# Kernel optimization log

Measured on AMD Instinct MI355X. Metric: run time of the kernel, lower is better.

## Reference

```python
import jax, jax.numpy as jnp
import numpy as np

PI = float(np.pi)
C64 = jnp.complex64

# ---- gate matrices (PennyLane conventions) ----

def _rx(t):
    c = jnp.cos(t / 2); s = jnp.sin(t / 2)
    return jnp.array([[c, -1j * s], [-1j * s, c]]).astype(C64)

def _rz(t):
    return jnp.array([[jnp.exp(-0.5j * t), 0.0], [0.0, jnp.exp(0.5j * t)]]).astype(C64)

def _rot(phi, th, om):
    # Rot(phi, theta, omega) = RZ(omega) RY(theta) RZ(phi)
    c = jnp.cos(th / 2); s = jnp.sin(th / 2)
    return jnp.array([
        [jnp.exp(-0.5j * (phi + om)) * c, -jnp.exp(0.5j * (phi - om)) * s],
        [jnp.exp(-0.5j * (phi - om)) * s,  jnp.exp(0.5j * (phi + om)) * c],
    ]).astype(C64)

def _crx(t):
    c = jnp.cos(t / 2); s = jnp.sin(t / 2)
    return jnp.array([
        [1, 0, 0, 0],
        [0, 1, 0, 0],
        [0, 0, c, -1j * s],
        [0, 0, -1j * s, c],
    ]).astype(C64)

CNOT = jnp.array([[1, 0, 0, 0], [0, 1, 0, 0], [0, 0, 0, 1], [0, 0, 1, 0]], dtype=C64)

# ---- state-vector primitives (state shape (2,)*n) ----

def _ap1(psi, U, w):
    return jnp.moveaxis(jnp.tensordot(U, psi, axes=((1,), (w,))), 0, w)

def _ap2(psi, U, a, b):
    U = U.reshape(2, 2, 2, 2)
    return jnp.moveaxis(jnp.tensordot(U, psi, axes=((2, 3), (a, b))), (0, 1), (a, b))

def _expZ(psi, w):
    p = jnp.moveaxis(jnp.abs(psi) ** 2, w, 0)
    return (p[0] - p[1]).sum()

def _expX(psi, w):
    return jnp.real(jnp.sum(jnp.conj(psi) * jnp.flip(psi, axis=w)))

# wire pairs in initQKV_on_wires order
_PAIRS = [(0, 1), (1, 2), (2, 3), (3, 0), (0, 3), (1, 0), (2, 1), (3, 2)]

def _init_qkv(psi, rot_p, crx_p, off):
    for i, (a, b) in enumerate(_PAIRS):
        psi = _ap1(psi, _rot(rot_p[3 * i], rot_p[3 * i + 1], rot_p[3 * i + 2]), off + a)
        psi = _ap2(psi, _crx(crx_p[i]), off + a, off + b)
        psi = _ap2(psi, CNOT, off + a, off + b)
    return psi

def _sample(x, qr, qc, kr, kc, vr, vc):
    # qmha_score: 8-qubit circuit
    psi = jnp.zeros((2,) * 8, C64).at[(0,) * 8].set(1.0)
    for w in range(4):  # AngleEmbedding (RX) of xq
        psi = _ap1(psi, _rx(x[w]), w)
    psi = _init_qkv(psi, qr, qc, 0)
    for w in range(4):  # AngleEmbedding (RX) of xk (same x)
        psi = _ap1(psi, _rx(x[w]), w)
    psi = _init_qkv(psi, kr, kc, 4)
    for w in range(4):
        psi = _ap2(psi, CNOT, w, w + 4)
    z = jnp.stack([_expZ(psi, w) for w in range(4)])
    xm = jnp.stack([_expX(psi, w) for w in range(4)])
    score = jnp.sqrt(z * z + xm * xm)
    # qmha_value: 4-qubit circuit
    phi = jnp.zeros((2,) * 4, C64).at[(0,) * 4].set(1.0)
    for w in range(4):
        phi = _ap1(phi, _rx(x[w]), w)
    phi = _init_qkv(phi, vr, vc, 0)
    for w in range(4):
        phi = _ap1(phi, _rz(jnp.tanh(score[w]) * PI), w)
    for a, b in [(0, 1), (1, 2), (2, 3)]:
        phi = _ap2(phi, CNOT, a, b)
    zv = jnp.stack([_expZ(phi, w) for w in range(4)])
    xv = jnp.stack([_expX(phi, w) for w in range(4)])
    return jnp.concatenate([zv, xv])  # [8]


def setup_inputs() -> dict:
    key = jax.random.key(0)
    ks = jax.random.split(key, 12)
    B = 16384
    u = lambda k, n: jax.random.uniform(k, (n,), jnp.float32, -PI / 2, PI / 2)
    return {
        "x1": jax.random.normal(ks[0], (B, 96), jnp.float32),
        "pre_w": jax.random.normal(ks[1], (4, 96), jnp.float32) / np.sqrt(96.0),
        "pre_b": jnp.zeros((4,), jnp.float32),
        "q_rot": u(ks[2], 24),
        "k_rot": u(ks[3], 24),
        "v_rot": u(ks[4], 24),
        "q_crx": 0.1 * jax.random.normal(ks[5], (8,), jnp.float32),
        "k_crx": 0.1 * jax.random.normal(ks[6], (8,), jnp.float32),
        "v_crx": 0.1 * jax.random.normal(ks[7], (8,), jnp.float32),
        "ln_w": jnp.ones((8,), jnp.float32),
        "ln_b": jnp.zeros((8,), jnp.float32),
        "head_w": jax.random.normal(ks[8], (2, 8), jnp.float32) / np.sqrt(8.0),
        "head_b": jnp.zeros((2,), jnp.float32),
    }


def reference(x1, pre_w, pre_b, q_rot, k_rot, v_rot, q_crx, k_crx, v_crx,
              ln_w, ln_b, head_w, head_b):
    x = x1 @ pre_w.T + pre_b  # [B, 4] angles
    outs = jax.vmap(lambda xi: _sample(xi, q_rot, q_crx, k_rot, k_crx, v_rot, v_crx))(x)  # [B, 8]
    mu = outs.mean(-1, keepdims=True)
    var = outs.var(-1, keepdims=True)
    y = (outs - mu) / jnp.sqrt(var + 1e-5) * ln_w + ln_b  # LayerNorm(8)
    g = jax.nn.gelu(y, approximate=False)  # torch nn.GELU default = exact erf
    return g @ head_w.T + head_b  # [B, 2]
```

## Files before the change

kernel.cpp:

```cpp
#include <hip/hip_runtime.h>
#include <math.h>

#define PI_F 3.14159265358979323846f

struct c32 { float x, y; };

#define DPP_X1 0xB1
#define DPP_X2 0x4E
#define DPP_X3 0x1B

template<int CTRL>
__device__ __forceinline__ float dppf(float v){
  return __int_as_float(__builtin_amdgcn_update_dpp(
      0, __float_as_int(v), CTRL, 0xF, 0xF, true));
}

__device__ __forceinline__ float qred(float v){
  v += dppf<DPP_X1>(v);
  v += dppf<DPP_X2>(v);
  return v;
}

__device__ __forceinline__ float sel4(bool b0, bool b1,
                                      float v0, float v1, float v2, float v3){
  float lo = b0 ? v1 : v0;
  float hi = b0 ? v3 : v2;
  return b1 ? hi : lo;
}

__device__ __forceinline__ float fast_tanh(float x){
  float e = __expf(2.f * x);
  return 1.f - 2.f * __builtin_amdgcn_rcpf(e + 1.f);
}


template<int XM>
__device__ __forceinline__ void rot_lane(c32* a, float Ax, float Ay,
                                         float Cx, float Cy, float sgn){
  c32 r[4];
  #pragma unroll
  for (int k = 0; k < 4; k++){ r[k].x = dppf<XM>(a[k].x); r[k].y = dppf<XM>(a[k].y); }
  float Py = Ay * sgn, Qx = -Cx * sgn;
  #pragma unroll
  for (int k = 0; k < 4; k++){
    float nx = Ax*a[k].x - Py*a[k].y + Qx*r[k].x - Cy*r[k].y;
    float ny = Ax*a[k].y + Py*a[k].x + Qx*r[k].y + Cy*r[k].x;
    a[k].x = nx; a[k].y = ny;
  }
}

template<int MB>
__device__ __forceinline__ void rot_local(c32* a, float Ax, float Ay,
                                          float Cx, float Cy){
  #pragma unroll
  for (int k = 0; k < 4; k++){
    if (k & MB) continue;
    c32 u = a[k], v = a[k|MB];
    a[k].x    = Ax*u.x - Ay*u.y - Cx*v.x - Cy*v.y;
    a[k].y    = Ax*u.y + Ay*u.x - Cx*v.y + Cy*v.x;
    a[k|MB].x = Cx*u.x - Cy*u.y + Ax*v.x + Ay*v.y;
    a[k|MB].y = Cx*u.y + Cy*u.x + Ax*v.y - Ay*v.x;
  }
}

__device__ __forceinline__ void crx_pair(c32& u, c32& v, float c, float sn){
  c32 uo = u, vo = v;
  u.x = c*vo.x + sn*uo.y;  u.y = c*vo.y - sn*uo.x;
  v.x = c*uo.x + sn*vo.y;  v.y = c*uo.y - sn*vo.x;
}

template<int KM>
__device__ __forceinline__ void crx_lanectl_local(c32* a, float c, float sn, bool act){
  c32 n[4];
  #pragma unroll
  for (int k = 0; k < 4; k++){
    n[k].x = c*a[k^KM].x + sn*a[k].y;
    n[k].y = c*a[k^KM].y - sn*a[k].x;
  }
  #pragma unroll
  for (int k = 0; k < 4; k++){
    a[k].x = act ? n[k].x : a[k].x;
    a[k].y = act ? n[k].y : a[k].y;
  }
}

template<int XM, int K0, int K1>
__device__ __forceinline__ void crx_localctl_lane(c32* a, float c, float sn){
  float rx0 = dppf<XM>(a[K0].x), ry0 = dppf<XM>(a[K0].y);
  float rx1 = dppf<XM>(a[K1].x), ry1 = dppf<XM>(a[K1].y);
  float u0x = a[K0].x, u0y = a[K0].y, u1x = a[K1].x, u1y = a[K1].y;
  a[K0].x = c*rx0 + sn*u0y;  a[K0].y = c*ry0 - sn*u0x;
  a[K1].x = c*rx1 + sn*u1y;  a[K1].y = c*ry1 - sn*u1x;
}

template<int XM>
__device__ __forceinline__ void crx_lane_lane(c32* a, float c, float sn, bool act){
  #pragma unroll
  for (int k = 0; k < 4; k++){
    float rx = dppf<XM>(a[k].x), ry = dppf<XM>(a[k].y);
    float nx = c*rx + sn*a[k].y;
    float ny = c*ry - sn*a[k].x;
    a[k].x = act ? nx : a[k].x;
    a[k].y = act ? ny : a[k].y;
  }
}

__device__ __forceinline__ void sim4(c32* a, const float* __restrict__ gp,
                                     float sgnW0, float sgnW1, bool qb0, bool qb1){
  rot_lane<DPP_X2>(a, gp[0],  gp[1],  gp[2],  gp[3],  sgnW0);
  crx_lane_lane<DPP_X1>(a, gp[4], gp[5], qb1);
  rot_lane<DPP_X1>(a, gp[8],  gp[9],  gp[10], gp[11], sgnW1);
  crx_lanectl_local<2>(a, gp[12], gp[13], qb0);
  rot_local<2>(a, gp[16], gp[17], gp[18], gp[19]);
  crx_pair(a[2], a[3], gp[20], gp[21]);
  rot_local<1>(a, gp[24], gp[25], gp[26], gp[27]);
  crx_localctl_lane<DPP_X2,1,3>(a, gp[28], gp[29]);
  rot_lane<DPP_X2>(a, gp[32], gp[33], gp[34], gp[35], sgnW0);
  crx_lanectl_local<1>(a, gp[36], gp[37], qb1);
  rot_lane<DPP_X1>(a, gp[40], gp[41], gp[42], gp[43], sgnW1);
  crx_lane_lane<DPP_X2>(a, gp[44], gp[45], qb0);
  rot_local<2>(a, gp[48], gp[49], gp[50], gp[51]);
  crx_localctl_lane<DPP_X1,2,3>(a, gp[52], gp[53]);
  rot_local<1>(a, gp[56], gp[57], gp[58], gp[59]);
  crx_pair(a[1], a[3], gp[60], gp[61]);
}

__device__ __forceinline__ void build_rx4(c32* a, const float* cw, const float* sw,
                                          int q, bool qb0, bool qb1){
  float m01 = (qb1 ? sw[0] : cw[0]) * (qb0 ? sw[1] : cw[1]);
  float g0 = m01 * (cw[2]*cw[3]);
  float g1 = m01 * (cw[2]*sw[3]);
  float g2 = m01 * (sw[2]*cw[3]);
  float g3 = m01 * (sw[2]*sw[3]);
  float bx = (q == 0) ? 1.f : (q == 3) ? -1.f : 0.f;
  float by = (q == 1 || q == 2) ? -1.f : 0.f;
  a[0].x =  g0*bx;  a[0].y =  g0*by;
  a[1].x =  g1*by;  a[1].y = -g1*bx;
  a[2].x =  g2*by;  a[2].y = -g2*bx;
  a[3].x = -g3*bx;  a[3].y = -g3*by;
}

__device__ __forceinline__ void apply_rot_red16(c32* s, const int w,
                                                float Ax, float Ay, float Cx, float Cy){
  const int m = 8 >> w;
  #pragma unroll
  for (int i = 0; i < 16; i++){
    if (i & m) continue;
    c32 a = s[i], b = s[i | m];
    s[i].x     = Ax*a.x - Ay*a.y - Cx*b.x - Cy*b.y;
    s[i].y     = Ax*a.y + Ay*a.x - Cx*b.y + Cy*b.x;
    s[i | m].x = Cx*a.x - Cy*a.y + Ax*b.x + Ay*b.y;
    s[i | m].y = Cx*a.y + Cy*a.x + Ax*b.y - Ay*b.x;
  }
}

__device__ __forceinline__ void apply_crxnot16(c32* s, const int wa, const int wb,
                                               float c, float sn){
  const int ma = 8 >> wa, mb = 8 >> wb;
  #pragma unroll
  for (int i = 0; i < 16; i++){
    if (!(i & ma) || (i & mb)) continue;
    c32 u = s[i], v = s[i | mb];
    s[i]      = { c*v.x + sn*u.y, c*v.y - sn*u.x };
    s[i | mb] = { c*u.x + sn*v.y, c*u.y - sn*v.x };
  }
}

__global__ __launch_bounds__(64, 1) void qc_setup(
    const float* __restrict__ q_rot, const float* __restrict__ k_rot,
    const float* __restrict__ v_rot,
    const float* __restrict__ q_crx, const float* __restrict__ k_crx,
    const float* __restrict__ v_crx,
    float* __restrict__ ws){

  __shared__ float gates[3 * 64];
  const int t = threadIdx.x;

  if (t < 24){
    const int grp = t >> 3, g = t & 7;
    const float* rotp = grp == 0 ? q_rot : (grp == 1 ? k_rot : v_rot);
    const float* crxp = grp == 0 ? q_crx : (grp == 1 ? k_crx : v_crx);
    float phi = rotp[3*g], th = rotp[3*g+1], om = rotp[3*g+2];
    float c, s, ca, sa, cb, sb;
    __sincosf(0.5f*th,       &s,  &c);
    __sincosf(0.5f*(phi+om), &sa, &ca);
    __sincosf(0.5f*(phi-om), &sb, &cb);
    float cc, cs; __sincosf(0.5f*crxp[g], &cs, &cc);
    float* dst = &gates[64*grp + 8*g];
    dst[0] = c*ca; dst[1] = -c*sa; dst[2] = s*cb; dst[3] = -s*sb;
    dst[4] = cc;   dst[5] = cs;
    dst[6] = 0.f;  dst[7] = 0.f;
  }
  __syncthreads();

  c32 ks[16];
  #pragma unroll
  for (int i = 0; i < 16; i++) ks[i] = { 0.f, 0.f };
  ks[0] = { 1.f, 0.f };
  {
    constexpr int pa[8] = {0,1,2,3,0,1,2,3};
    constexpr int pb[8] = {1,2,3,0,3,0,1,2};
    #pragma unroll
    for (int g = 0; g < 8; g++){
      const float* qq = &gates[64 + 8*g];
      apply_rot_red16(ks, pa[g], qq[0], qq[1], qq[2], qq[3]);
      apply_crxnot16(ks, pa[g], pb[g], qq[4], qq[5]);
    }
  }
  float cxk[4];
  #pragma unroll
  for (int w = 0; w < 4; w++){
    const int m = 8 >> w;
    float r = 0.f;
    #pragma unroll
    for (int i = 0; i < 16; i++){
      if (i & m) continue;
      r += ks[i].x*ks[i|m].x + ks[i].y*ks[i|m].y;
    }
    cxk[w] = 2.f * r;
  }

  ws[t]      = gates[t];
  ws[64 + t] = gates[128 + t];
  if (t < 4) ws[128 + t] = cxk[t];
}

__global__ __launch_bounds__(256, 1) void qc_main(
    const float* __restrict__ x1,
    const float* __restrict__ pre_w, const float* __restrict__ pre_b,
    const float* __restrict__ gws,
    const float* __restrict__ ln_w, const float* __restrict__ ln_b,
    const float* __restrict__ head_w, const float* __restrict__ head_b,
    float* __restrict__ out, int B){

  __shared__ float pw[4][100];
  __shared__ float scr[32][9];

  const int t    = threadIdx.x;
  const int lane = t & 63;
  const int wid  = t >> 6;
  const bool qrole = (wid & 1) == 0;
  const int sm   = (wid >> 1) * 16 + (lane >> 2);
  const int q    = lane & 3;
  const bool qb0 = (q & 1) != 0;
  const bool qb1 = (q & 2) != 0;
  const int sid  = blockIdx.x * 32 + sm;
  const int sidc = (sid < B) ? sid : (B - 1);

  if (t < 96){
    float4 v = ((const float4*)pre_w)[t];
    int r = t / 24, c4 = (t % 24) * 4;
    pw[r][c4+0] = v.x; pw[r][c4+1] = v.y; pw[r][c4+2] = v.z; pw[r][c4+3] = v.w;
  }
  __syncthreads();

  float xw[4];
  {
    float a0 = 0.f, a1 = 0.f, a2 = 0.f, a3 = 0.f;
    const float4* xrow = (const float4*)(x1 + (size_t)sidc * 96 + 24*q);
    #pragma unroll
    for (int j = 0; j < 6; j++){
      float4 xv = xrow[j];
      const int c = 24*q + 4*j;
      float4 w0 = *(const float4*)&pw[0][c];
      float4 w1 = *(const float4*)&pw[1][c];
      float4 w2 = *(const float4*)&pw[2][c];
      float4 w3 = *(const float4*)&pw[3][c];
      a0 += xv.x*w0.x + xv.y*w0.y + xv.z*w0.z + xv.w*w0.w;
      a1 += xv.x*w1.x + xv.y*w1.y + xv.z*w1.z + xv.w*w1.w;
      a2 += xv.x*w2.x + xv.y*w2.y + xv.z*w2.z + xv.w*w2.w;
      a3 += xv.x*w3.x + xv.y*w3.y + xv.z*w3.z + xv.w*w3.w;
    }
    xw[0] = qred(a0) + pre_b[0];
    xw[1] = qred(a1) + pre_b[1];
    xw[2] = qred(a2) + pre_b[2];
    xw[3] = qred(a3) + pre_b[3];
  }

  float cw[4], sw[4];
  #pragma unroll
  for (int w = 0; w < 4; w++) __sincosf(0.5f*xw[w], &sw[w], &cw[w]);

  const float sgnW0 = qb1 ? -1.f : 1.f;
  const float sgnW1 = qb0 ? -1.f : 1.f;

  c32 a[4];
  build_rx4(a, cw, sw, q, qb0, qb1);

  float o0, o1, o2, o3;

  if (qrole){
    sim4(a, gws, sgnW0, sgnW1, qb0, qb1);

    float p0 = a[0].x*a[0].x + a[0].y*a[0].y;
    float p1 = a[1].x*a[1].x + a[1].y*a[1].y;
    float p2 = a[2].x*a[2].x + a[2].y*a[2].y;
    float p3 = a[3].x*a[3].x + a[3].y*a[3].y;
    float psum = p0 + p1 + p2 + p3;

    float sz2 = p0 + p1 - p2 - p3;
    float sx2 = 2.f*(a[0].x*a[2].x + a[0].y*a[2].y + a[1].x*a[3].x + a[1].y*a[3].y);
    float sy2 = 2.f*(a[0].x*a[2].y - a[0].y*a[2].x + a[1].x*a[3].y - a[1].y*a[3].x);
    float sz3 = p0 - p1 + p2 - p3;
    float sx3 = 2.f*(a[0].x*a[1].x + a[0].y*a[1].y + a[2].x*a[3].x + a[2].y*a[3].y);
    float sy3 = 2.f*(a[0].x*a[1].y - a[0].y*a[1].x + a[2].x*a[3].y - a[2].y*a[3].x);

    c32 r[4];
    #pragma unroll
    for (int k = 0; k < 4; k++){ r[k].x = dppf<DPP_X2>(a[k].x); r[k].y = dppf<DPP_X2>(a[k].y); }
    float sx0 = a[0].x*r[0].x + a[0].y*r[0].y + a[1].x*r[1].x + a[1].y*r[1].y
              + a[2].x*r[2].x + a[2].y*r[2].y + a[3].x*r[3].x + a[3].y*r[3].y;
    float sy0 = (a[0].x*r[0].y - a[0].y*r[0].x + a[1].x*r[1].y - a[1].y*r[1].x
               + a[2].x*r[2].y - a[2].y*r[2].x + a[3].x*r[3].y - a[3].y*r[3].x) * sgnW0;
    float sz0 = sgnW0 * psum;

    #pragma unroll
    for (int k = 0; k < 4; k++){ r[k].x = dppf<DPP_X1>(a[k].x); r[k].y = dppf<DPP_X1>(a[k].y); }
    float sx1 = a[0].x*r[0].x + a[0].y*r[0].y + a[1].x*r[1].x + a[1].y*r[1].y
              + a[2].x*r[2].x + a[2].y*r[2].y + a[3].x*r[3].x + a[3].y*r[3].y;
    float sy1 = (a[0].x*r[0].y - a[0].y*r[0].x + a[1].x*r[1].y - a[1].y*r[1].x
               + a[2].x*r[2].y - a[2].y*r[2].x + a[3].x*r[3].y - a[3].y*r[3].x) * sgnW1;
    float sz1 = sgnW1 * psum;

    sz0 = qred(sz0); sx0 = qred(sx0); sy0 = qred(sy0);
    sz1 = qred(sz1); sx1 = qred(sx1); sy1 = qred(sy1);
    sz2 = qred(sz2); sx2 = qred(sx2); sy2 = qred(sy2);
    sz3 = qred(sz3); sx3 = qred(sx3); sy3 = qred(sy3);

    float szq = sel4(qb0, qb1, sz0, sz1, sz2, sz3);
    float sxq = sel4(qb0, qb1, sx0, sx1, sx2, sx3);
    float syq = sel4(qb0, qb1, sy0, sy1, sy2, sy3);
    float swq = sel4(qb0, qb1, sw[0], sw[1], sw[2], sw[3]);
    float cwq = sel4(qb0, qb1, cw[0], cw[1], cw[2], cw[3]);
    float cxkq = sel4(qb0, qb1, gws[128], gws[129], gws[130], gws[131]);

    float cth = 1.f - 2.f*swq*swq;
    float sth = 2.f*swq*cwq;
    float z   = cth*szq + sth*syq;
    float xm  = sxq * cxkq;
    float score = sqrtf(z*z + xm*xm);
    float th = fast_tanh(score) * PI_F;
    float srv, crv; __sincosf(0.5f*th, &srv, &crv);
    scr[sm][2*q]     = crv;
    scr[sm][2*q + 1] = srv;
  } else {
    sim4(a, gws + 64, sgnW0, sgnW1, qb0, qb1);

    float p0 = a[0].x*a[0].x + a[0].y*a[0].y;
    float p1 = a[1].x*a[1].x + a[1].y*a[1].y;
    float p2 = a[2].x*a[2].x + a[2].y*a[2].y;
    float p3 = a[3].x*a[3].x + a[3].y*a[3].y;
    float psum = p0 + p1 + p2 + p3;
    float sgn01 = sgnW0 * sgnW1;
    o0 = qred(sgnW0 * psum);
    o1 = qred(sgn01 * psum);
    o2 = qred(sgn01 * (p0 + p1 - p2 - p3));
    o3 = qred(sgn01 * (p0 - p1 - p2 + p3));
  }

  __syncthreads();

  if (!qrole){
    float c0 = scr[sm][0], s0 = scr[sm][1];
    float c1 = scr[sm][2], s1 = scr[sm][3];
    float c2 = scr[sm][4], s2 = scr[sm][5];
    float c3 = scr[sm][6], s3 = scr[sm][7];

    float c01m = c0*c1 - s0*s1, c01p = c0*c1 + s0*s1;
    float s01p = c0*s1 + s0*c1, s01m = c0*s1 - s0*c1;
    bool selq = qb0 != qb1;
    float phx = selq ? c01p : c01m;
    float phm = selq ? s01m : s01p;
    float phy = qb0 ? phm : -phm;
    float c23m = c2*c3 - s2*s3, c23p = c2*c3 + s2*s3;
    float s23p = c2*s3 + s2*c3, s23m = c2*s3 - s2*c3;
    c32 P[4] = { {c23m, -s23p}, {c23p, s23m}, {c23p, -s23m}, {c23m, s23p} };
    #pragma unroll
    for (int k = 0; k < 4; k++){
      c32 b = { a[k].x*phx - a[k].y*phy, a[k].x*phy + a[k].y*phx };
      a[k].x = b.x*P[k].x - b.y*P[k].y;
      a[k].y = b.x*P[k].y + b.y*P[k].x;
    }

    c32 r[4];
    #pragma unroll
    for (int k = 0; k < 4; k++){ r[k].x = dppf<DPP_X3>(a[k].x); r[k].y = dppf<DPP_X3>(a[k].y); }
    float s4 = a[0].x*r[0].x + a[0].y*r[0].y + a[1].x*r[1].x + a[1].y*r[1].y
             + a[2].x*r[2].x + a[2].y*r[2].y + a[3].x*r[3].x + a[3].y*r[3].y;
    #pragma unroll
    for (int k = 0; k < 4; k++){ r[k].x = dppf<DPP_X1>(a[k].x); r[k].y = dppf<DPP_X1>(a[k].y); }
    float s5 = a[0].x*r[2].x + a[0].y*r[2].y + a[1].x*r[3].x + a[1].y*r[3].y
             + a[2].x*r[0].x + a[2].y*r[0].y + a[3].x*r[1].x + a[3].y*r[1].y;
    float s6 = 2.f*(a[0].x*a[3].x + a[0].y*a[3].y + a[1].x*a[2].x + a[1].y*a[2].y);
    float s7 = 2.f*(a[0].x*a[1].x + a[0].y*a[1].y + a[2].x*a[3].x + a[2].y*a[3].y);
    float o4 = qred(s4), o5 = qred(s5), o6 = qred(s6), o7 = qred(s7);

    float o[8] = { o0, o1, o2, o3, o4, o5, o6, o7 };
    float mu = 0.f;
    #pragma unroll
    for (int j = 0; j < 8; j++) mu += o[j];
    mu *= 0.125f;
    float var = 0.f;
    #pragma unroll
    for (int j = 0; j < 8; j++){ float d = o[j] - mu; var += d*d; }
    var *= 0.125f;
    float inv = rsqrtf(var + 1e-5f);
    float h0 = head_b[0], h1 = head_b[1];
    #pragma unroll
    for (int j = 0; j < 8; j++){
      float y = (o[j] - mu) * inv * ln_w[j] + ln_b[j];
      float u = 0.7978845608f * (y + 0.044715f*y*y*y);
      float g = 0.5f * y * (1.f + fast_tanh(u));
      h0 += g * head_w[j];
      h1 += g * head_w[8 + j];
    }

    if (q == 0 && sid < B){
      float2 r2; r2.x = h0; r2.y = h1;
      ((float2*)out)[sid] = r2;
    }
  }
}

extern "C" void kernel_launch(void* const* d_in, const int* in_sizes, int n_in,
                              void* d_out, int out_size, void* d_ws, size_t ws_size,
                              hipStream_t stream) {
  const float* x1     = (const float*)d_in[0];
  const float* pre_w  = (const float*)d_in[1];
  const float* pre_b  = (const float*)d_in[2];
  const float* q_rot  = (const float*)d_in[3];
  const float* k_rot  = (const float*)d_in[4];
  const float* v_rot  = (const float*)d_in[5];
  const float* q_crx  = (const float*)d_in[6];
  const float* k_crx  = (const float*)d_in[7];
  const float* v_crx  = (const float*)d_in[8];
  const float* ln_w   = (const float*)d_in[9];
  const float* ln_b   = (const float*)d_in[10];
  const float* head_w = (const float*)d_in[11];
  const float* head_b = (const float*)d_in[12];
  float* out = (float*)d_out;
  float* ws  = (float*)d_ws;
  (void)ws_size; (void)n_in; (void)out_size;

  const int B = in_sizes[0] / 96;
  const int nb = (B + 31) / 32;

  qc_setup<<<1, 64, 0, stream>>>(q_rot, k_rot, v_rot, q_crx, k_crx, v_crx, ws);
  qc_main<<<nb, 256, 0, stream>>>(x1, pre_w, pre_b, ws,
                                  ln_w, ln_b, head_w, head_b, out, B);
}
```

Baseline: 89.37 us.

## Fuse gate setup kernel into main kernel and recompute K expectation per block

Removes the separate single-block setup kernel. Each main-kernel block now computes the gate cos/sin coefficients into shared memory, and the q-role warps re-simulate the K-only circuit with the existing 4-lane sim4 routine to get the X expectations. The x1 row loads are hoisted ahead of the first barrier so they overlap with the pre_w and gate setup. This saves one launch and its dependency, at the cost of redundant per-block trig and an extra sim4 pass on the q-role warps.

```diff
diff --git a/kernel.cpp b/kernel.cpp
--- a/kernel.cpp
+++ b/kernel.cpp
@@ -105,7 +105,7 @@
   }
 }
 
-__device__ __forceinline__ void sim4(c32* a, const float* __restrict__ gp,
+__device__ __forceinline__ void sim4(c32* a, const float* gp,
                                      float sgnW0, float sgnW1, bool qb0, bool qb1){
   rot_lane<DPP_X2>(a, gp[0],  gp[1],  gp[2],  gp[3],  sgnW0);
   crx_lane_lane<DPP_X1>(a, gp[4], gp[5], qb1);
@@ -140,100 +140,19 @@
   a[3].x = -g3*bx;  a[3].y = -g3*by;
 }
 
-__device__ __forceinline__ void apply_rot_red16(c32* s, const int w,
-                                                float Ax, float Ay, float Cx, float Cy){
-  const int m = 8 >> w;
-  #pragma unroll
-  for (int i = 0; i < 16; i++){
-    if (i & m) continue;
-    c32 a = s[i], b = s[i | m];
-    s[i].x     = Ax*a.x - Ay*a.y - Cx*b.x - Cy*b.y;
-    s[i].y     = Ax*a.y + Ay*a.x - Cx*b.y + Cy*b.x;
-    s[i | m].x = Cx*a.x - Cy*a.y + Ax*b.x + Ay*b.y;
-    s[i | m].y = Cx*a.y + Cy*a.x + Ax*b.y - Ay*b.x;
-  }
-}
-
-__device__ __forceinline__ void apply_crxnot16(c32* s, const int wa, const int wb,
-                                               float c, float sn){
-  const int ma = 8 >> wa, mb = 8 >> wb;
-  #pragma unroll
-  for (int i = 0; i < 16; i++){
-    if (!(i & ma) || (i & mb)) continue;
-    c32 u = s[i], v = s[i | mb];
-    s[i]      = { c*v.x + sn*u.y, c*v.y - sn*u.x };
-    s[i | mb] = { c*u.x + sn*v.y, c*u.y - sn*v.x };
-  }
-}
-
-__global__ __launch_bounds__(64, 1) void qc_setup(
+__global__ __launch_bounds__(256, 1) void qc_main(
+    const float* __restrict__ x1,
+    const float* __restrict__ pre_w, const float* __restrict__ pre_b,
     const float* __restrict__ q_rot, const float* __restrict__ k_rot,
     const float* __restrict__ v_rot,
     const float* __restrict__ q_crx, const float* __restrict__ k_crx,
     const float* __restrict__ v_crx,
-    float* __restrict__ ws){
-
-  __shared__ float gates[3 * 64];
-  const int t = threadIdx.x;
-
-  if (t < 24){
-    const int grp = t >> 3, g = t & 7;
-    const float* rotp = grp == 0 ? q_rot : (grp == 1 ? k_rot : v_rot);
-    const float* crxp = grp == 0 ? q_crx : (grp == 1 ? k_crx : v_crx);
-    float phi = rotp[3*g], th = rotp[3*g+1], om = rotp[3*g+2];
-    float c, s, ca, sa, cb, sb;
-    __sincosf(0.5f*th,       &s,  &c);
-    __sincosf(0.5f*(phi+om), &sa, &ca);
-    __sincosf(0.5f*(phi-om), &sb, &cb);
-    float cc, cs; __sincosf(0.5f*crxp[g], &cs, &cc);
-    float* dst = &gates[64*grp + 8*g];
-    dst[0] = c*ca; dst[1] = -c*sa; dst[2] = s*cb; dst[3] = -s*sb;
-    dst[4] = cc;   dst[5] = cs;
-    dst[6] = 0.f;  dst[7] = 0.f;
-  }
-  __syncthreads();
-
-  c32 ks[16];
-  #pragma unroll
-  for (int i = 0; i < 16; i++) ks[i] = { 0.f, 0.f };
-  ks[0] = { 1.f, 0.f };
-  {
-    constexpr int pa[8] = {0,1,2,3,0,1,2,3};
-    constexpr int pb[8] = {1,2,3,0,3,0,1,2};
-    #pragma unroll
-    for (int g = 0; g < 8; g++){
-      const float* qq = &gates[64 + 8*g];
-      apply_rot_red16(ks, pa[g], qq[0], qq[1], qq[2], qq[3]);
-      apply_crxnot16(ks, pa[g], pb[g], qq[4], qq[5]);
-    }
-  }
-  float cxk[4];
-  #pragma unroll
-  for (int w = 0; w < 4; w++){
-    const int m = 8 >> w;
-    float r = 0.f;
-    #pragma unroll
-    for (int i = 0; i < 16; i++){
-      if (i & m) continue;
-      r += ks[i].x*ks[i|m].x + ks[i].y*ks[i|m].y;
-    }
-    cxk[w] = 2.f * r;
-  }
-
-  ws[t]      = gates[t];
-  ws[64 + t] = gates[128 + t];
-  if (t < 4) ws[128 + t] = cxk[t];
-}
-
-__global__ __launch_bounds__(256, 1) void qc_main(
-    const float* __restrict__ x1,
-    const float* __restrict__ pre_w, const float* __restrict__ pre_b,
-    const float* __restrict__ gws,
     const float* __restrict__ ln_w, const float* __restrict__ ln_b,
     const float* __restrict__ head_w, const float* __restrict__ head_b,
     float* __restrict__ out, int B){
 
   __shared__ float pw[4][100];
+  __shared__ float gl[192];
   __shared__ float scr[32][9];
 
   const int t    = threadIdx.x;
@@ -247,20 +166,43 @@
   const int sid  = blockIdx.x * 32 + sm;
   const int sidc = (sid < B) ? sid : (B - 1);
 
+  float4 xr[6];
+  {
+    const float4* xrow = (const float4*)(x1 + (size_t)sidc * 96 + 24*q);
+    #pragma unroll
+    for (int j = 0; j < 6; j++) xr[j] = xrow[j];
+  }
+
   if (t < 96){
     float4 v = ((const float4*)pre_w)[t];
     int r = t / 24, c4 = (t % 24) * 4;
     pw[r][c4+0] = v.x; pw[r][c4+1] = v.y; pw[r][c4+2] = v.z; pw[r][c4+3] = v.w;
   }
+
+  if (t >= 96 && t < 120){
+    const int u = t - 96;
+    const int grp = u >> 3, g = u & 7;
+    const float* rotp = grp == 0 ? q_rot : (grp == 1 ? k_rot : v_rot);
+    const float* crxp = grp == 0 ? q_crx : (grp == 1 ? k_crx : v_crx);
+    float phi = rotp[3*g], th = rotp[3*g+1], om = rotp[3*g+2];
+    float c, s, ca, sa, cb, sb;
+    __sincosf(0.5f*th,       &s,  &c);
+    __sincosf(0.5f*(phi+om), &sa, &ca);
+    __sincosf(0.5f*(phi-om), &sb, &cb);
+    float cc, cs; __sincosf(0.5f*crxp[g], &cs, &cc);
+    float* dst = &gl[64*grp + 8*g];
+    dst[0] = c*ca; dst[1] = -c*sa; dst[2] = s*cb; dst[3] = -s*sb;
+    dst[4] = cc;   dst[5] = cs;
+    dst[6] = 0.f;  dst[7] = 0.f;
+  }
   __syncthreads();
 
   float xw[4];
   {
     float a0 = 0.f, a1 = 0.f, a2 = 0.f, a3 = 0.f;
-    const float4* xrow = (const float4*)(x1 + (size_t)sidc * 96 + 24*q);
     #pragma unroll
     for (int j = 0; j < 6; j++){
-      float4 xv = xrow[j];
+      float4 xv = xr[j];
       const int c = 24*q + 4*j;
       float4 w0 = *(const float4*)&pw[0][c];
       float4 w1 = *(const float4*)&pw[1][c];
@@ -290,7 +232,7 @@
   float o0, o1, o2, o3;
 
   if (qrole){
-    sim4(a, gws, sgnW0, sgnW1, qb0, qb1);
+    sim4(a, &gl[0], sgnW0, sgnW1, qb0, qb1);
 
     float p0 = a[0].x*a[0].x + a[0].y*a[0].y;
     float p1 = a[1].x*a[1].x + a[1].y*a[1].y;
@@ -332,7 +274,26 @@
     float syq = sel4(qb0, qb1, sy0, sy1, sy2, sy3);
     float swq = sel4(qb0, qb1, sw[0], sw[1], sw[2], sw[3]);
     float cwq = sel4(qb0, qb1, cw[0], cw[1], cw[2], cw[3]);
-    float cxkq = sel4(qb0, qb1, gws[128], gws[129], gws[130], gws[131]);
+
+    c32 b[4];
+    b[0].x = (q == 0) ? 1.f : 0.f; b[0].y = 0.f;
+    b[1].x = 0.f; b[1].y = 0.f;
+    b[2].x = 0.f; b[2].y = 0.f;
+    b[3].x = 0.f; b[3].y = 0.f;
+    sim4(b, &gl[64], sgnW0, sgnW1, qb0, qb1);
+
+    float kx2 = 2.f*(b[0].x*b[2].x + b[0].y*b[2].y + b[1].x*b[3].x + b[1].y*b[3].y);
+    float kx3 = 2.f*(b[0].x*b[1].x + b[0].y*b[1].y + b[2].x*b[3].x + b[2].y*b[3].y);
+    #pragma unroll
+    for (int k = 0; k < 4; k++){ r[k].x = dppf<DPP_X2>(b[k].x); r[k].y = dppf<DPP_X2>(b[k].y); }
+    float kx0 = b[0].x*r[0].x + b[0].y*r[0].y + b[1].x*r[1].x + b[1].y*r[1].y
+              + b[2].x*r[2].x + b[2].y*r[2].y + b[3].x*r[3].x + b[3].y*r[3].y;
+    #pragma unroll
+    for (int k = 0; k < 4; k++){ r[k].x = dppf<DPP_X1>(b[k].x); r[k].y = dppf<DPP_X1>(b[k].y); }
+    float kx1 = b[0].x*r[0].x + b[0].y*r[0].y + b[1].x*r[1].x + b[1].y*r[1].y
+              + b[2].x*r[2].x + b[2].y*r[2].y + b[3].x*r[3].x + b[3].y*r[3].y;
+    kx0 = qred(kx0); kx1 = qred(kx1); kx2 = qred(kx2); kx3 = qred(kx3);
+    float cxkq = sel4(qb0, qb1, kx0, kx1, kx2, kx3);
 
     float cth = 1.f - 2.f*swq*swq;
     float sth = 2.f*swq*cwq;
@@ -344,7 +305,7 @@
     scr[sm][2*q]     = crv;
     scr[sm][2*q + 1] = srv;
   } else {
-    sim4(a, gws + 64, sgnW0, sgnW1, qb0, qb1);
+    sim4(a, &gl[128], sgnW0, sgnW1, qb0, qb1);
 
     float p0 = a[0].x*a[0].x + a[0].y*a[0].y;
     float p1 = a[1].x*a[1].x + a[1].y*a[1].y;
@@ -377,9 +338,9 @@
     c32 P[4] = { {c23m, -s23p}, {c23p, s23m}, {c23p, -s23m}, {c23m, s23p} };
     #pragma unroll
     for (int k = 0; k < 4; k++){
-      c32 b = { a[k].x*phx - a[k].y*phy, a[k].x*phy + a[k].y*phx };
-      a[k].x = b.x*P[k].x - b.y*P[k].y;
-      a[k].y = b.x*P[k].y + b.y*P[k].x;
+      c32 bb = { a[k].x*phx - a[k].y*phy, a[k].x*phy + a[k].y*phx };
+      a[k].x = bb.x*P[k].x - bb.y*P[k].y;
+      a[k].y = bb.x*P[k].y + bb.y*P[k].x;
     }
 
     c32 r[4];
@@ -439,13 +400,12 @@
   const float* head_w = (const float*)d_in[11];
   const float* head_b = (const float*)d_in[12];
   float* out = (float*)d_out;
-  float* ws  = (float*)d_ws;
-  (void)ws_size; (void)n_in; (void)out_size;
+  (void)d_ws; (void)ws_size; (void)n_in; (void)out_size;
 
   const int B = in_sizes[0] / 96;
   const int nb = (B + 31) / 32;
 
-  qc_setup<<<1, 64, 0, stream>>>(q_rot, k_rot, v_rot, q_crx, k_crx, v_crx, ws);
-  qc_main<<<nb, 256, 0, stream>>>(x1, pre_w, pre_b, ws,
+  qc_main<<<nb, 256, 0, stream>>>(x1, pre_w, pre_b,
+                                  q_rot, k_rot, v_rot, q_crx, k_crx, v_crx,
                                   ln_w, ln_b, head_w, head_b, out, B);
 }
```

Result: faster. 86.33 us (-3.4%).
